# Kernel optimization log

Hardware: AMD Instinct MI355X
Metric: run time of the kernel (lower is better)

Reference implementation:

```python
import jax, jax.numpy as jnp
import numpy as np

B, L, D, H = 64, 2048, 128, 4
A = 128          # atom_dim
M = 16           # num_prototypes
V = 100000       # vocab_size
NNZ = 262144     # total atoms across batch
HD = D // H      # head_dim
GAMMA, BETA, TAU = 0.3, 1.0, 1.0


def setup_inputs() -> dict:
    key = jax.random.key(0)
    ks = jax.random.split(key, 14)
    token_states = jax.random.normal(ks[0], (B, L, D), dtype=jnp.float32)
    query_ids = jax.random.randint(ks[1], (NNZ,), 0, V, dtype=jnp.int64)
    inner = jnp.sort(jax.random.randint(ks[2], (B - 1,), 0, NNZ, dtype=jnp.int64))
    query_offs = jnp.concatenate([jnp.zeros(1, jnp.int64), inner,
                                  jnp.full((1,), NNZ, jnp.int64)])
    atom_emb = jax.random.normal(ks[3], (V, A), dtype=jnp.float32) * 0.02
    phi_logits = jax.random.normal(ks[4], (M, V), dtype=jnp.float32) * 0.02
    W_A = jax.random.normal(ks[5], (A, A), dtype=jnp.float32) * (A ** -0.5)
    W_B = jax.random.normal(ks[6], (A, A), dtype=jnp.float32) * (A ** -0.5)
    W_val = jax.random.normal(ks[7], (HD, A), dtype=jnp.float32) * (A ** -0.5)
    b_val = jax.random.normal(ks[8], (HD,), dtype=jnp.float32) * 0.01
    W_gate = jax.random.normal(ks[9], (H, D), dtype=jnp.float32) * (D ** -0.5)
    b_gate = jax.random.normal(ks[10], (H,), dtype=jnp.float32) * 0.01
    W_out = jax.random.normal(ks[11], (D, D), dtype=jnp.float32) * (D ** -0.5)
    b_out = jax.random.normal(ks[12], (D,), dtype=jnp.float32) * 0.01
    size_w = jax.random.normal(ks[13], (2,), dtype=jnp.float32) * 0.01
    return dict(token_states=token_states, query_ids=query_ids, query_offs=query_offs,
                atom_emb=atom_emb, phi_logits=phi_logits, W_A=W_A, W_B=W_B,
                W_val=W_val, b_val=b_val, W_gate=W_gate, b_gate=b_gate,
                W_out=W_out, b_out=b_out, size_w=size_w)


def reference(token_states, query_ids, query_offs, atom_emb, phi_logits,
              W_A, W_B, W_val, b_val, W_gate, b_gate, W_out, b_out, size_w):
    nB, nL, nD = token_states.shape
    nnz = query_ids.shape[0]
    # segment id for each CSR entry: b s.t. offs[b] <= i < offs[b+1]
    seg = jnp.searchsorted(query_offs[1:], jnp.arange(nnz), side='right')
    # Phi(S) = sum of atom embeddings per set  -> (B, A)
    PhiQ = jax.ops.segment_sum(atom_emb[query_ids], seg, num_segments=nB)
    sizeQ = (query_offs[1:] - query_offs[:-1]).astype(jnp.float32)  # (B,)
    # prototype memberships and features
    p = jax.nn.sigmoid(phi_logits)        # (M, V)
    PhiP = p @ atom_emb                   # (M, A)
    sizeP = p.sum(axis=-1)                # (M,)
    # E[Delta(S,p)] = |S| + |p|_1 - 2 * sum_{u in S} p_u  -> (B, M)
    sum_p_S = jax.ops.segment_sum(p[:, query_ids].T, seg, num_segments=nB)
    delta = sizeQ[:, None] + sizeP[None, :] - 2.0 * sum_p_S
    # attention scores over prototypes
    AQ = PhiQ @ W_A.T                     # (B, A)
    BP = PhiP @ W_B.T                     # (M, A)
    dot = AQ @ BP.T                       # (B, M)
    size_term = size_w[0] * sizeQ[:, None] + size_w[1] * sizeP[None, :]
    scores = -GAMMA * delta + BETA * dot + size_term
    attn = jax.nn.softmax(scores / max(1e-6, TAU), axis=1)   # (B, M)
    Vp = PhiP @ W_val.T + b_val           # (M, HD)
    Z = attn @ Vp                         # (B, HD), shared across heads
    # token->set gates and mixing
    gates = jax.nn.softmax(token_states @ W_gate.T + b_gate, axis=-1)  # (B, L, H)
    mixed = (gates[..., None] * Z[:, None, None, :]).reshape(nB, nL, nD)
    return mixed @ W_out.T + b_out
```

## Files before the change

kernel.cpp:

```cpp
#include <hip/hip_runtime.h>
#include <hip/hip_bf16.h>

constexpr int Bn = 64;
constexpr int Ln = 2048;
constexpr int Dn = 128;
constexpr int Hn = 4;
constexpr int An = 128;
constexpr int Mn = 16;
constexpr int Vn = 100000;
constexpr int HDn = 32;
constexpr float GAMMA = 0.3f;
constexpr float BETA = 1.0f;

constexpr size_t OFF_PHIP  = 0;
constexpr size_t OFF_SIZEP = 2048;
constexpr size_t OFF_PHIQ  = 2064;
constexpr size_t OFF_SUMPS = 10256;
constexpr size_t OFF_C     = 11280;
constexpr size_t OFF_PT    = 44048;
constexpr size_t WS_FLOATS_NEEDED = OFF_PT + (size_t)Vn * 16;

__global__ __launch_bounds__(256) void k_phip(const float* __restrict__ phi,
                                              const float* __restrict__ E,
                                              float* __restrict__ PhiP,
                                              float* __restrict__ sizeP,
                                              float* __restrict__ pT,
                                              int write_pT) {
    __shared__ float pv[64 * 16];
    __shared__ float szl[Mn];
    const int t = threadIdx.x;
    const int a4 = t & 31;
    const int g = t >> 5;
    const int vloc = t >> 2;
    const int mbase = 4 * (t & 3);

    if (t < Mn) szl[t] = 0.f;

    float4 acc0 = make_float4(0.f, 0.f, 0.f, 0.f);
    float4 acc1 = make_float4(0.f, 0.f, 0.f, 0.f);
    float4 szacc = make_float4(0.f, 0.f, 0.f, 0.f);

    for (int v0 = blockIdx.x * 64; v0 < Vn; v0 += gridDim.x * 64) {
        __syncthreads();
        const int v = v0 + vloc;
        float4 pj = make_float4(0.f, 0.f, 0.f, 0.f);
        if (v < Vn) {
            const float x0 = phi[(size_t)(mbase + 0) * Vn + v];
            const float x1 = phi[(size_t)(mbase + 1) * Vn + v];
            const float x2 = phi[(size_t)(mbase + 2) * Vn + v];
            const float x3 = phi[(size_t)(mbase + 3) * Vn + v];
            pj.x = 1.f / (1.f + __expf(-x0));
            pj.y = 1.f / (1.f + __expf(-x1));
            pj.z = 1.f / (1.f + __expf(-x2));
            pj.w = 1.f / (1.f + __expf(-x3));
        }
        *(float4*)&pv[4 * t] = pj;
        szacc.x += pj.x; szacc.y += pj.y; szacc.z += pj.z; szacc.w += pj.w;
        if (write_pT && v < Vn) {
            *(float4*)&pT[(size_t)v * 16 + mbase] = pj;
        }
        __syncthreads();
        const int vmax = min(64, Vn - v0);
#pragma unroll 8
        for (int vv = 0; vv < vmax; ++vv) {
            const float4 e = *(const float4*)&E[(size_t)(v0 + vv) * An + a4 * 4];
            const float2 pm = *(const float2*)&pv[vv * 16 + g * 2];
            acc0.x += pm.x * e.x; acc0.y += pm.x * e.y; acc0.z += pm.x * e.z; acc0.w += pm.x * e.w;
            acc1.x += pm.y * e.x; acc1.y += pm.y * e.y; acc1.z += pm.y * e.z; acc1.w += pm.y * e.w;
        }
    }
    {
        float* d0 = &PhiP[(size_t)(2 * g + 0) * An + a4 * 4];
        float* d1 = &PhiP[(size_t)(2 * g + 1) * An + a4 * 4];
        atomicAdd(d0 + 0, acc0.x); atomicAdd(d0 + 1, acc0.y);
        atomicAdd(d0 + 2, acc0.z); atomicAdd(d0 + 3, acc0.w);
        atomicAdd(d1 + 0, acc1.x); atomicAdd(d1 + 1, acc1.y);
        atomicAdd(d1 + 2, acc1.z); atomicAdd(d1 + 3, acc1.w);
    }
    atomicAdd(&szl[mbase + 0], szacc.x);
    atomicAdd(&szl[mbase + 1], szacc.y);
    atomicAdd(&szl[mbase + 2], szacc.z);
    atomicAdd(&szl[mbase + 3], szacc.w);
    __syncthreads();
    if (t < Mn) atomicAdd(&sizeP[t], szl[t]);
}

__global__ __launch_bounds__(256) void k_phiq(const int* __restrict__ qid,
                                              const int* __restrict__ offs,
                                              const float* __restrict__ E,
                                              const float* __restrict__ phi,
                                              const float* __restrict__ pT,
                                              int usepT,
                                              float* __restrict__ PhiQ,
                                              float* __restrict__ sumpS) {
    const int b = blockIdx.y;
    const int s0 = offs[b], s1 = offs[b + 1];
    const int len = s1 - s0;
    const int nsplit = (int)gridDim.x;
    const int chunk = (len + nsplit - 1) / nsplit;
    const int start = s0 + (int)blockIdx.x * chunk;
    const int end = min(start + chunk, s1);
    const int t = threadIdx.x;

    __shared__ float phl[8 * 128];
    __shared__ float sP[Mn];
    if (t < Mn) sP[t] = 0.f;

    {
        const int a4 = t & 31, sub = t >> 5;
        float4 acc = make_float4(0.f, 0.f, 0.f, 0.f);
        const float4* E4 = (const float4*)E;
        int i = start + sub;
        for (; i + 24 < end; i += 32) {
            const int q0 = qid[i], q1 = qid[i + 8], q2 = qid[i + 16], q3 = qid[i + 24];
            const float4 e0 = E4[(size_t)q0 * 32 + a4];
            const float4 e1 = E4[(size_t)q1 * 32 + a4];
            const float4 e2 = E4[(size_t)q2 * 32 + a4];
            const float4 e3 = E4[(size_t)q3 * 32 + a4];
            acc.x += e0.x + e1.x + e2.x + e3.x;
            acc.y += e0.y + e1.y + e2.y + e3.y;
            acc.z += e0.z + e1.z + e2.z + e3.z;
            acc.w += e0.w + e1.w + e2.w + e3.w;
        }
        for (; i < end; i += 8) {
            const float4 e = E4[(size_t)qid[i] * 32 + a4];
            acc.x += e.x; acc.y += e.y; acc.z += e.z; acc.w += e.w;
        }
        *(float4*)&phl[sub * 128 + a4 * 4] = acc;
    }
    __syncthreads();
    if (t < 128) {
        float s = 0.f;
#pragma unroll
        for (int k = 0; k < 8; ++k) s += phl[k * 128 + t];
        atomicAdd(&PhiQ[(size_t)b * An + t], s);
    }

    float4 acc = make_float4(0.f, 0.f, 0.f, 0.f);
    const int m4 = t & 3, io = t >> 2;
    if (usepT) {
        const float4* pT4 = (const float4*)pT;
        int i = start + io;
        for (; i + 192 < end; i += 256) {
            const int q0 = qid[i], q1 = qid[i + 64], q2 = qid[i + 128], q3 = qid[i + 192];
            const float4 p0 = pT4[(size_t)q0 * 4 + m4];
            const float4 p1 = pT4[(size_t)q1 * 4 + m4];
            const float4 p2 = pT4[(size_t)q2 * 4 + m4];
            const float4 p3 = pT4[(size_t)q3 * 4 + m4];
            acc.x += p0.x + p1.x + p2.x + p3.x;
            acc.y += p0.y + p1.y + p2.y + p3.y;
            acc.z += p0.z + p1.z + p2.z + p3.z;
            acc.w += p0.w + p1.w + p2.w + p3.w;
        }
        for (; i < end; i += 64) {
            const float4 p = pT4[(size_t)qid[i] * 4 + m4];
            acc.x += p.x; acc.y += p.y; acc.z += p.z; acc.w += p.w;
        }
    } else {
        for (int i = start + io; i < end; i += 64) {
            const int q = qid[i];
            acc.x += 1.f / (1.f + __expf(-phi[(size_t)(m4 * 4 + 0) * Vn + q]));
            acc.y += 1.f / (1.f + __expf(-phi[(size_t)(m4 * 4 + 1) * Vn + q]));
            acc.z += 1.f / (1.f + __expf(-phi[(size_t)(m4 * 4 + 2) * Vn + q]));
            acc.w += 1.f / (1.f + __expf(-phi[(size_t)(m4 * 4 + 3) * Vn + q]));
        }
    }
#pragma unroll
    for (int off = 32; off >= 4; off >>= 1) {
        acc.x += __shfl_xor(acc.x, off);
        acc.y += __shfl_xor(acc.y, off);
        acc.z += __shfl_xor(acc.z, off);
        acc.w += __shfl_xor(acc.w, off);
    }
    if ((t & 63) < 4) {
        atomicAdd(&sP[m4 * 4 + 0], acc.x);
        atomicAdd(&sP[m4 * 4 + 1], acc.y);
        atomicAdd(&sP[m4 * 4 + 2], acc.z);
        atomicAdd(&sP[m4 * 4 + 3], acc.w);
    }
    __syncthreads();
    if (t < Mn) atomicAdd(&sumpS[(size_t)b * Mn + t], sP[t]);
}

__global__ __launch_bounds__(128) void k_small(const float* __restrict__ PhiP,
                                               const float* __restrict__ sizeP,
                                               const float* __restrict__ PhiQ,
                                               const float* __restrict__ sumpS,
                                               const int* __restrict__ offs,
                                               const float* __restrict__ W_A,
                                               const float* __restrict__ W_B,
                                               const float* __restrict__ W_val,
                                               const float* __restrict__ b_val,
                                               const float* __restrict__ W_out,
                                               const float* __restrict__ size_w,
                                               float* __restrict__ Cws) {
    const int b = blockIdx.x;
    const int i = threadIdx.x;
    __shared__ float BP[Mn * An];
    __shared__ float Vp[Mn * HDn];
    __shared__ float AQs[An];
    __shared__ float sc[Mn];
    __shared__ float attn[Mn];
    __shared__ float Zs[HDn];

    {
        const float4* wa = (const float4*)(W_A + (size_t)i * An);
        const float4* pq = (const float4*)(PhiQ + (size_t)b * An);
        float aq = 0.f;
        for (int q = 0; q < An / 4; ++q) {
            const float4 w = wa[q], p = pq[q];
            aq += w.x * p.x + w.y * p.y + w.z * p.z + w.w * p.w;
        }
        AQs[i] = aq;
    }
    {
        const float4* wb = (const float4*)(W_B + (size_t)i * An);
        for (int m = 0; m < Mn; ++m) {
            const float4* pp = (const float4*)(PhiP + (size_t)m * An);
            float s = 0.f;
            for (int q = 0; q < An / 4; ++q) {
                const float4 w = wb[q], p = pp[q];
                s += w.x * p.x + w.y * p.y + w.z * p.z + w.w * p.w;
            }
            BP[m * An + i] = s;
        }
    }
    if (i < HDn) {
        const float4* wv = (const float4*)(W_val + (size_t)i * An);
        for (int m = 0; m < Mn; ++m) {
            const float4* pp = (const float4*)(PhiP + (size_t)m * An);
            float s = 0.f;
            for (int q = 0; q < An / 4; ++q) {
                const float4 w = wv[q], p = pp[q];
                s += w.x * p.x + w.y * p.y + w.z * p.z + w.w * p.w;
            }
            Vp[m * HDn + i] = s + b_val[i];
        }
    }
    __syncthreads();

    const float szQ = (float)(offs[b + 1] - offs[b]);
    if (i < Mn) {
        float d = 0.f;
        for (int a = 0; a < An; ++a) d += AQs[a] * BP[i * An + a];
        const float delta = szQ + sizeP[i] - 2.f * sumpS[(size_t)b * Mn + i];
        sc[i] = -GAMMA * delta + BETA * d + size_w[0] * szQ + size_w[1] * sizeP[i];
    }
    __syncthreads();
    if (i < Mn) {
        float mx = sc[0];
        for (int m = 1; m < Mn; ++m) mx = fmaxf(mx, sc[m]);
        float sum = 0.f;
        for (int m = 0; m < Mn; ++m) sum += __expf(sc[m] - mx);
        attn[i] = __expf(sc[i] - mx) / sum;
    }
    __syncthreads();
    if (i < HDn) {
        float z = 0.f;
        for (int m = 0; m < Mn; ++m) z += attn[m] * Vp[m * HDn + i];
        Zs[i] = z;
    }
    __syncthreads();
    {
        const float* wo = W_out + (size_t)i * Dn;
#pragma unroll
        for (int h = 0; h < Hn; ++h) {
            float c = 0.f;
#pragma unroll
            for (int j = 0; j < HDn; ++j) c += Zs[j] * wo[h * HDn + j];
            Cws[((size_t)b * Hn + h) * Dn + i] = c;
        }
    }
}

__global__ __launch_bounds__(256) void k_out(const float* __restrict__ ts,
                                             const float* __restrict__ W_gate,
                                             const float* __restrict__ b_gate,
                                             const float* __restrict__ b_out,
                                             const float* __restrict__ Cws,
                                             float* __restrict__ out) {
    constexpr int CHUNK = 128;
    const int b = blockIdx.y;
    const int t = threadIdx.x;
    __shared__ float4 WgS[Hn * 32];
    __shared__ float4 CS[Hn * 32];
    __shared__ float4 boS[32];
    __shared__ float bgS[Hn];
    if (t < 128) WgS[t] = ((const float4*)W_gate)[t];
    else CS[t - 128] = ((const float4*)(Cws + (size_t)b * Hn * Dn))[t - 128];
    if (t < 32) boS[t] = ((const float4*)b_out)[t];
    if (t >= 64 && t < 64 + Hn) bgS[t - 64] = b_gate[t - 64];
    __syncthreads();

    const int sl = t & 31;
    const int tg = t >> 5;
    const size_t rowbase = (size_t)b * Ln + (size_t)blockIdx.x * CHUNK;
    const float4* x4 = (const float4*)ts + rowbase * 32;
    float4* o4 = (float4*)out + rowbase * 32;

    const float4 w0 = WgS[0 * 32 + sl], w1 = WgS[1 * 32 + sl];
    const float4 w2 = WgS[2 * 32 + sl], w3 = WgS[3 * 32 + sl];
    const float4 c0 = CS[0 * 32 + sl], c1 = CS[1 * 32 + sl];
    const float4 c2 = CS[2 * 32 + sl], c3 = CS[3 * 32 + sl];
    const float4 bo = boS[sl];
    const float bg0 = bgS[0], bg1 = bgS[1], bg2 = bgS[2], bg3 = bgS[3];

    for (int it = 0; it < CHUNK / 8; ++it) {
        const int tok = it * 8 + tg;
        const float4 x = x4[(size_t)tok * 32 + sl];
        float a0 = x.x * w0.x + x.y * w0.y + x.z * w0.z + x.w * w0.w;
        float a1 = x.x * w1.x + x.y * w1.y + x.z * w1.z + x.w * w1.w;
        float a2 = x.x * w2.x + x.y * w2.y + x.z * w2.z + x.w * w2.w;
        float a3 = x.x * w3.x + x.y * w3.y + x.z * w3.z + x.w * w3.w;
#pragma unroll
        for (int off = 16; off > 0; off >>= 1) {
            a0 += __shfl_xor(a0, off);
            a1 += __shfl_xor(a1, off);
            a2 += __shfl_xor(a2, off);
            a3 += __shfl_xor(a3, off);
        }
        a0 += bg0; a1 += bg1; a2 += bg2; a3 += bg3;
        const float mx = fmaxf(fmaxf(a0, a1), fmaxf(a2, a3));
        const float e0 = __expf(a0 - mx), e1 = __expf(a1 - mx);
        const float e2 = __expf(a2 - mx), e3 = __expf(a3 - mx);
        const float inv = 1.f / (e0 + e1 + e2 + e3);
        const float g0 = e0 * inv, g1 = e1 * inv, g2 = e2 * inv, g3 = e3 * inv;
        float4 o = bo;
        o.x += g0 * c0.x + g1 * c1.x + g2 * c2.x + g3 * c3.x;
        o.y += g0 * c0.y + g1 * c1.y + g2 * c2.y + g3 * c3.y;
        o.z += g0 * c0.z + g1 * c1.z + g2 * c2.z + g3 * c3.z;
        o.w += g0 * c0.w + g1 * c1.w + g2 * c2.w + g3 * c3.w;
        o4[(size_t)tok * 32 + sl] = o;
    }
}

extern "C" void kernel_launch(void* const* d_in, const int* in_sizes, int n_in,
                              void* d_out, int out_size, void* d_ws, size_t ws_size,
                              hipStream_t stream) {
    const float* ts     = (const float*)d_in[0];
    const int*   qid    = (const int*)d_in[1];
    const int*   offs   = (const int*)d_in[2];
    const float* E      = (const float*)d_in[3];
    const float* phi    = (const float*)d_in[4];
    const float* W_A    = (const float*)d_in[5];
    const float* W_B    = (const float*)d_in[6];
    const float* W_val  = (const float*)d_in[7];
    const float* b_val  = (const float*)d_in[8];
    const float* W_gate = (const float*)d_in[9];
    const float* b_gate = (const float*)d_in[10];
    const float* W_out  = (const float*)d_in[11];
    const float* b_out  = (const float*)d_in[12];
    const float* size_w = (const float*)d_in[13];
    float* out = (float*)d_out;
    float* ws  = (float*)d_ws;

    float* PhiP  = ws + OFF_PHIP;
    float* sizeP = ws + OFF_SIZEP;
    float* PhiQ  = ws + OFF_PHIQ;
    float* sumpS = ws + OFF_SUMPS;
    float* Cws   = ws + OFF_C;
    float* pT    = ws + OFF_PT;
    const int usepT = (ws_size >= WS_FLOATS_NEEDED * sizeof(float)) ? 1 : 0;

    hipMemsetAsync(ws, 0, OFF_C * sizeof(float), stream);
    k_phip<<<dim3(512), dim3(256), 0, stream>>>(phi, E, PhiP, sizeP, pT, usepT);
    k_phiq<<<dim3(64, Bn), dim3(256), 0, stream>>>(qid, offs, E, phi, pT, usepT, PhiQ, sumpS);
    k_small<<<dim3(Bn), dim3(128), 0, stream>>>(PhiP, sizeP, PhiQ, sumpS, offs,
                                                W_A, W_B, W_val, b_val, W_out, size_w, Cws);
    k_out<<<dim3(Ln / 128, Bn), dim3(256), 0, stream>>>(ts, W_gate, b_gate, b_out, Cws, out);
}
```

Baseline: 322.4 us.

## Restructure PhiP kernel: one 128-vocab tile per block, all prototypes per thread

The prototype-embedding kernel now launches one block per 128-row vocab tile instead of a grid-stride loop over 512 blocks. Each thread accumulates all 16 prototypes against one float4 of the embedding row, so each embedding load is reused 16 times instead of 2. Partial sums are reduced through shuffles and shared memory, then written to global memory with atomics. This cuts redundant embedding reads and per-iteration barriers, but uses 64 accumulator registers per thread and issues far more global atomics from about 782 blocks.

```diff
diff --git a/kernel.cpp b/kernel.cpp
--- a/kernel.cpp
+++ b/kernel.cpp
@@ -20,68 +20,127 @@
 constexpr size_t OFF_PT    = 44048;
 constexpr size_t WS_FLOATS_NEEDED = OFF_PT + (size_t)Vn * 16;
 
+__device__ __forceinline__ float sigm(float x) { return 1.f / (1.f + __expf(-x)); }
+
 __global__ __launch_bounds__(256) void k_phip(const float* __restrict__ phi,
                                               const float* __restrict__ E,
                                               float* __restrict__ PhiP,
                                               float* __restrict__ sizeP,
                                               float* __restrict__ pT,
                                               int write_pT) {
-    __shared__ float pv[64 * 16];
+    __shared__ float pv[128 * 16];
+    __shared__ float4 red[4 * Mn * 32];
     __shared__ float szl[Mn];
     const int t = threadIdx.x;
+    const int v0 = (int)blockIdx.x * 128;
+    const int nvalid = min(128, Vn - v0);
+
+    if (t < Mn) szl[t] = 0.f;
+    __syncthreads();
+
+    {
+        const int vl = t >> 1;
+        const int mb = 8 * (t & 1);
+        float4 p0 = make_float4(0.f, 0.f, 0.f, 0.f);
+        float4 p1 = make_float4(0.f, 0.f, 0.f, 0.f);
+        if (vl < nvalid) {
+            const int v = v0 + vl;
+            p0.x = sigm(phi[(size_t)(mb + 0) * Vn + v]);
+            p0.y = sigm(phi[(size_t)(mb + 1) * Vn + v]);
+            p0.z = sigm(phi[(size_t)(mb + 2) * Vn + v]);
+            p0.w = sigm(phi[(size_t)(mb + 3) * Vn + v]);
+            p1.x = sigm(phi[(size_t)(mb + 4) * Vn + v]);
+            p1.y = sigm(phi[(size_t)(mb + 5) * Vn + v]);
+            p1.z = sigm(phi[(size_t)(mb + 6) * Vn + v]);
+            p1.w = sigm(phi[(size_t)(mb + 7) * Vn + v]);
+            if (write_pT) {
+                *(float4*)&pT[(size_t)v * 16 + mb + 0] = p0;
+                *(float4*)&pT[(size_t)v * 16 + mb + 4] = p1;
+            }
+            atomicAdd(&szl[mb + 0], p0.x); atomicAdd(&szl[mb + 1], p0.y);
+            atomicAdd(&szl[mb + 2], p0.z); atomicAdd(&szl[mb + 3], p0.w);
+            atomicAdd(&szl[mb + 4], p1.x); atomicAdd(&szl[mb + 5], p1.y);
+            atomicAdd(&szl[mb + 6], p1.z); atomicAdd(&szl[mb + 7], p1.w);
+        }
+        *(float4*)&pv[vl * 16 + mb + 0] = p0;
+        *(float4*)&pv[vl * 16 + mb + 4] = p1;
+    }
+    __syncthreads();
+
     const int a4 = t & 31;
-    const int g = t >> 5;
-    const int vloc = t >> 2;
-    const int mbase = 4 * (t & 3);
-
-    if (t < Mn) szl[t] = 0.f;
-
-    float4 acc0 = make_float4(0.f, 0.f, 0.f, 0.f);
-    float4 acc1 = make_float4(0.f, 0.f, 0.f, 0.f);
-    float4 szacc = make_float4(0.f, 0.f, 0.f, 0.f);
-
-    for (int v0 = blockIdx.x * 64; v0 < Vn; v0 += gridDim.x * 64) {
-        __syncthreads();
-        const int v = v0 + vloc;
-        float4 pj = make_float4(0.f, 0.f, 0.f, 0.f);
-        if (v < Vn) {
-            const float x0 = phi[(size_t)(mbase + 0) * Vn + v];
-            const float x1 = phi[(size_t)(mbase + 1) * Vn + v];
-            const float x2 = phi[(size_t)(mbase + 2) * Vn + v];
-            const float x3 = phi[(size_t)(mbase + 3) * Vn + v];
-            pj.x = 1.f / (1.f + __expf(-x0));
-            pj.y = 1.f / (1.f + __expf(-x1));
-            pj.z = 1.f / (1.f + __expf(-x2));
-            pj.w = 1.f / (1.f + __expf(-x3));
-        }
-        *(float4*)&pv[4 * t] = pj;
-        szacc.x += pj.x; szacc.y += pj.y; szacc.z += pj.z; szacc.w += pj.w;
-        if (write_pT && v < Vn) {
-            *(float4*)&pT[(size_t)v * 16 + mbase] = pj;
-        }
-        __syncthreads();
-        const int vmax = min(64, Vn - v0);
-#pragma unroll 8
-        for (int vv = 0; vv < vmax; ++vv) {
-            const float4 e = *(const float4*)&E[(size_t)(v0 + vv) * An + a4 * 4];
-            const float2 pm = *(const float2*)&pv[vv * 16 + g * 2];
-            acc0.x += pm.x * e.x; acc0.y += pm.x * e.y; acc0.z += pm.x * e.z; acc0.w += pm.x * e.w;
-            acc1.x += pm.y * e.x; acc1.y += pm.y * e.y; acc1.z += pm.y * e.z; acc1.w += pm.y * e.w;
-        }
-    }
-    {
-        float* d0 = &PhiP[(size_t)(2 * g + 0) * An + a4 * 4];
-        float* d1 = &PhiP[(size_t)(2 * g + 1) * An + a4 * 4];
-        atomicAdd(d0 + 0, acc0.x); atomicAdd(d0 + 1, acc0.y);
-        atomicAdd(d0 + 2, acc0.z); atomicAdd(d0 + 3, acc0.w);
-        atomicAdd(d1 + 0, acc1.x); atomicAdd(d1 + 1, acc1.y);
-        atomicAdd(d1 + 2, acc1.z); atomicAdd(d1 + 3, acc1.w);
-    }
-    atomicAdd(&szl[mbase + 0], szacc.x);
-    atomicAdd(&szl[mbase + 1], szacc.y);
-    atomicAdd(&szl[mbase + 2], szacc.z);
-    atomicAdd(&szl[mbase + 3], szacc.w);
-    __syncthreads();
+    const int sub = t >> 5;
+    float4 acc[Mn];
+#pragma unroll
+    for (int m = 0; m < Mn; ++m) acc[m] = make_float4(0.f, 0.f, 0.f, 0.f);
+
+    const float4* E4 = (const float4*)E + (size_t)v0 * 32 + a4;
+    if (nvalid == 128) {
+#pragma unroll 4
+        for (int v = sub; v < 128; v += 8) {
+            const float4 e = E4[(size_t)v * 32];
+            const float4 q0 = *(const float4*)&pv[v * 16 + 0];
+            const float4 q1 = *(const float4*)&pv[v * 16 + 4];
+            const float4 q2 = *(const float4*)&pv[v * 16 + 8];
+            const float4 q3 = *(const float4*)&pv[v * 16 + 12];
+            acc[0].x += q0.x * e.x; acc[0].y += q0.x * e.y; acc[0].z += q0.x * e.z; acc[0].w += q0.x * e.w;
+            acc[1].x += q0.y * e.x; acc[1].y += q0.y * e.y; acc[1].z += q0.y * e.z; acc[1].w += q0.y * e.w;
+            acc[2].x += q0.z * e.x; acc[2].y += q0.z * e.y; acc[2].z += q0.z * e.z; acc[2].w += q0.z * e.w;
+            acc[3].x += q0.w * e.x; acc[3].y += q0.w * e.y; acc[3].z += q0.w * e.z; acc[3].w += q0.w * e.w;
+            acc[4].x += q1.x * e.x; acc[4].y += q1.x * e.y; acc[4].z += q1.x * e.z; acc[4].w += q1.x * e.w;
+            acc[5].x += q1.y * e.x; acc[5].y += q1.y * e.y; acc[5].z += q1.y * e.z; acc[5].w += q1.y * e.w;
+            acc[6].x += q1.z * e.x; acc[6].y += q1.z * e.y; acc[6].z += q1.z * e.z; acc[6].w += q1.z * e.w;
+            acc[7].x += q1.w * e.x; acc[7].y += q1.w * e.y; acc[7].z += q1.w * e.z; acc[7].w += q1.w * e.w;
+            acc[8].x += q2.x * e.x; acc[8].y += q2.x * e.y; acc[8].z += q2.x * e.z; acc[8].w += q2.x * e.w;
+            acc[9].x += q2.y * e.x; acc[9].y += q2.y * e.y; acc[9].z += q2.y * e.z; acc[9].w += q2.y * e.w;
+            acc[10].x += q2.z * e.x; acc[10].y += q2.z * e.y; acc[10].z += q2.z * e.z; acc[10].w += q2.z * e.w;
+            acc[11].x += q2.w * e.x; acc[11].y += q2.w * e.y; acc[11].z += q2.w * e.z; acc[11].w += q2.w * e.w;
+            acc[12].x += q3.x * e.x; acc[12].y += q3.x * e.y; acc[12].z += q3.x * e.z; acc[12].w += q3.x * e.w;
+            acc[13].x += q3.y * e.x; acc[13].y += q3.y * e.y; acc[13].z += q3.y * e.z; acc[13].w += q3.y * e.w;
+            acc[14].x += q3.z * e.x; acc[14].y += q3.z * e.y; acc[14].z += q3.z * e.z; acc[14].w += q3.z * e.w;
+            acc[15].x += q3.w * e.x; acc[15].y += q3.w * e.y; acc[15].z += q3.w * e.z; acc[15].w += q3.w * e.w;
+        }
+    } else {
+        for (int v = sub; v < nvalid; v += 8) {
+            const float4 e = E4[(size_t)v * 32];
+#pragma unroll
+            for (int m = 0; m < Mn; ++m) {
+                const float pm = pv[v * 16 + m];
+                acc[m].x += pm * e.x; acc[m].y += pm * e.y;
+                acc[m].z += pm * e.z; acc[m].w += pm * e.w;
+            }
+        }
+    }
+    __syncthreads();
+
+#pragma unroll
+    for (int m = 0; m < Mn; ++m) {
+        acc[m].x += __shfl_xor(acc[m].x, 32);
+        acc[m].y += __shfl_xor(acc[m].y, 32);
+        acc[m].z += __shfl_xor(acc[m].z, 32);
+        acc[m].w += __shfl_xor(acc[m].w, 32);
+    }
+    const int lane = t & 63, wv = t >> 6;
+    if (lane < 32) {
+#pragma unroll
+        for (int m = 0; m < Mn; ++m)
+            red[(wv * Mn + m) * 32 + a4] = acc[m];
+    }
+    __syncthreads();
+
+#pragma unroll
+    for (int r = 0; r < 2; ++r) {
+        const int idx = t + r * 256;
+        const int m = idx >> 5, a = idx & 31;
+        const float4 s0 = red[(0 * Mn + m) * 32 + a];
+        const float4 s1 = red[(1 * Mn + m) * 32 + a];
+        const float4 s2 = red[(2 * Mn + m) * 32 + a];
+        const float4 s3 = red[(3 * Mn + m) * 32 + a];
+        float* dst = &PhiP[(size_t)m * An + a * 4];
+        atomicAdd(dst + 0, s0.x + s1.x + s2.x + s3.x);
+        atomicAdd(dst + 1, s0.y + s1.y + s2.y + s3.y);
+        atomicAdd(dst + 2, s0.z + s1.z + s2.z + s3.z);
+        atomicAdd(dst + 3, s0.w + s1.w + s2.w + s3.w);
+    }
     if (t < Mn) atomicAdd(&sizeP[t], szl[t]);
 }
 
@@ -159,10 +218,10 @@
     } else {
         for (int i = start + io; i < end; i += 64) {
             const int q = qid[i];
-            acc.x += 1.f / (1.f + __expf(-phi[(size_t)(m4 * 4 + 0) * Vn + q]));
-            acc.y += 1.f / (1.f + __expf(-phi[(size_t)(m4 * 4 + 1) * Vn + q]));
-            acc.z += 1.f / (1.f + __expf(-phi[(size_t)(m4 * 4 + 2) * Vn + q]));
-            acc.w += 1.f / (1.f + __expf(-phi[(size_t)(m4 * 4 + 3) * Vn + q]));
+            acc.x += sigm(phi[(size_t)(m4 * 4 + 0) * Vn + q]);
+            acc.y += sigm(phi[(size_t)(m4 * 4 + 1) * Vn + q]);
+            acc.z += sigm(phi[(size_t)(m4 * 4 + 2) * Vn + q]);
+            acc.w += sigm(phi[(size_t)(m4 * 4 + 3) * Vn + q]);
         }
     }
 #pragma unroll
@@ -363,7 +422,7 @@
     const int usepT = (ws_size >= WS_FLOATS_NEEDED * sizeof(float)) ? 1 : 0;
 
     hipMemsetAsync(ws, 0, OFF_C * sizeof(float), stream);
-    k_phip<<<dim3(512), dim3(256), 0, stream>>>(phi, E, PhiP, sizeP, pT, usepT);
+    k_phip<<<dim3((Vn + 127) / 128), dim3(256), 0, stream>>>(phi, E, PhiP, sizeP, pT, usepT);
     k_phiq<<<dim3(64, Bn), dim3(256), 0, stream>>>(qid, offs, E, phi, pT, usepT, PhiQ, sumpS);
     k_small<<<dim3(Bn), dim3(128), 0, stream>>>(PhiP, sizeP, PhiQ, sumpS, offs,
                                                 W_A, W_B, W_val, b_val, W_out, size_w, Cws);
```

Result: slower. 347.3 us (+7.7%).

## Split PhiP into sigmoid-transpose pass and register-tiled GEMV with partial reduction

Applied to the files above, without the earlier changes.

The fused sigmoid+PhiP kernel becomes three kernels. k_pt computes sigmoid and writes the transposed p table plus sizeP. k_phip streams atom_emb once, keeping all 16 prototype accumulators in registers with software prefetch, and writes per-block partials. k_red reduces those partials, replacing the many global atomics of the old kernel. This costs extra launches, heavy register use, and an 8 MB partial buffer write and read; an atomic path is kept if the workspace is too small.

```diff
diff --git a/kernel.cpp b/kernel.cpp
--- a/kernel.cpp
+++ b/kernel.cpp
@@ -12,20 +12,147 @@
 constexpr float GAMMA = 0.3f;
 constexpr float BETA = 1.0f;
 
+constexpr int PHIP_BLOCKS = 1024;
+
 constexpr size_t OFF_PHIP  = 0;
 constexpr size_t OFF_SIZEP = 2048;
 constexpr size_t OFF_PHIQ  = 2064;
 constexpr size_t OFF_SUMPS = 10256;
 constexpr size_t OFF_C     = 11280;
 constexpr size_t OFF_PT    = 44048;
-constexpr size_t WS_FLOATS_NEEDED = OFF_PT + (size_t)Vn * 16;
-
-__global__ __launch_bounds__(256) void k_phip(const float* __restrict__ phi,
-                                              const float* __restrict__ E,
-                                              float* __restrict__ PhiP,
-                                              float* __restrict__ sizeP,
-                                              float* __restrict__ pT,
-                                              int write_pT) {
+constexpr size_t OFF_PART  = OFF_PT + (size_t)Vn * 16;
+constexpr size_t WS_FLOATS_PT   = OFF_PART;
+constexpr size_t WS_FLOATS_PART = OFF_PART + (size_t)PHIP_BLOCKS * Mn * An;
+
+__device__ __forceinline__ float sigm(float x) { return 1.f / (1.f + __expf(-x)); }
+
+__global__ __launch_bounds__(256) void k_pt(const float* __restrict__ phi,
+                                            float* __restrict__ pT,
+                                            float* __restrict__ sizeP) {
+    __shared__ float szl[Mn];
+    const int t = threadIdx.x;
+    if (t < Mn) szl[t] = 0.f;
+    __syncthreads();
+    const int v = (int)blockIdx.x * 256 + t;
+    if (v < Vn) {
+        float p[Mn];
+#pragma unroll
+        for (int m = 0; m < Mn; ++m) p[m] = sigm(phi[(size_t)m * Vn + v]);
+        float4* dst = (float4*)&pT[(size_t)v * 16];
+        dst[0] = make_float4(p[0], p[1], p[2], p[3]);
+        dst[1] = make_float4(p[4], p[5], p[6], p[7]);
+        dst[2] = make_float4(p[8], p[9], p[10], p[11]);
+        dst[3] = make_float4(p[12], p[13], p[14], p[15]);
+#pragma unroll
+        for (int m = 0; m < Mn; ++m) atomicAdd(&szl[m], p[m]);
+    }
+    __syncthreads();
+    if (t < Mn) atomicAdd(&sizeP[t], szl[t]);
+}
+
+__global__ __launch_bounds__(256, 4) void k_phip(const float* __restrict__ E,
+                                                 const float* __restrict__ pT,
+                                                 float* __restrict__ PhiP,
+                                                 float* __restrict__ part,
+                                                 int mode) {
+    const int t = threadIdx.x;
+    const int wv = t >> 6, lane = t & 63;
+    const int c = lane & 31;
+    const int rh = lane >> 5;
+    const int W = (int)gridDim.x * 4;
+    const int w = (int)blockIdx.x * 4 + wv;
+    constexpr int NP = Vn / 2;
+
+    const float4* E4 = (const float4*)E;
+    const float4* P4 = (const float4*)pT;
+
+    float4 acc[Mn];
+#pragma unroll
+    for (int m = 0; m < Mn; ++m) acc[m] = make_float4(0.f, 0.f, 0.f, 0.f);
+
+    int i = w;
+    float4 e_n = make_float4(0.f, 0.f, 0.f, 0.f);
+    float4 pf_n0 = e_n, pf_n1 = e_n, pf_n2 = e_n, pf_n3 = e_n;
+    if (i < NP) {
+        const size_t vr = (size_t)(2 * i + rh);
+        e_n = E4[vr * 32 + c];
+        pf_n0 = P4[vr * 4 + 0]; pf_n1 = P4[vr * 4 + 1];
+        pf_n2 = P4[vr * 4 + 2]; pf_n3 = P4[vr * 4 + 3];
+    }
+    while (i < NP) {
+        const float4 e = e_n;
+        const float4 f0 = pf_n0, f1 = pf_n1, f2 = pf_n2, f3 = pf_n3;
+        const int in = i + W;
+        if (in < NP) {
+            const size_t vr = (size_t)(2 * in + rh);
+            e_n = E4[vr * 32 + c];
+            pf_n0 = P4[vr * 4 + 0]; pf_n1 = P4[vr * 4 + 1];
+            pf_n2 = P4[vr * 4 + 2]; pf_n3 = P4[vr * 4 + 3];
+        }
+        float pm[Mn];
+        pm[0] = f0.x; pm[1] = f0.y; pm[2] = f0.z; pm[3] = f0.w;
+        pm[4] = f1.x; pm[5] = f1.y; pm[6] = f1.z; pm[7] = f1.w;
+        pm[8] = f2.x; pm[9] = f2.y; pm[10] = f2.z; pm[11] = f2.w;
+        pm[12] = f3.x; pm[13] = f3.y; pm[14] = f3.z; pm[15] = f3.w;
+#pragma unroll
+        for (int m = 0; m < Mn; ++m) {
+            acc[m].x += pm[m] * e.x; acc[m].y += pm[m] * e.y;
+            acc[m].z += pm[m] * e.z; acc[m].w += pm[m] * e.w;
+        }
+        i = in;
+    }
+
+#pragma unroll
+    for (int m = 0; m < Mn; ++m) {
+        acc[m].x += __shfl_xor(acc[m].x, 32);
+        acc[m].y += __shfl_xor(acc[m].y, 32);
+        acc[m].z += __shfl_xor(acc[m].z, 32);
+        acc[m].w += __shfl_xor(acc[m].w, 32);
+    }
+    __shared__ float4 red[4 * Mn * 32];
+    if (lane < 32) {
+#pragma unroll
+        for (int m = 0; m < Mn; ++m) red[(wv * Mn + m) * 32 + c] = acc[m];
+    }
+    __syncthreads();
+#pragma unroll
+    for (int r = 0; r < 2; ++r) {
+        const int idx = t + r * 256;
+        const int m = idx >> 5, a = idx & 31;
+        const float4 s0 = red[(0 * Mn + m) * 32 + a];
+        const float4 s1 = red[(1 * Mn + m) * 32 + a];
+        const float4 s2 = red[(2 * Mn + m) * 32 + a];
+        const float4 s3 = red[(3 * Mn + m) * 32 + a];
+        const float4 s = make_float4(s0.x + s1.x + s2.x + s3.x,
+                                     s0.y + s1.y + s2.y + s3.y,
+                                     s0.z + s1.z + s2.z + s3.z,
+                                     s0.w + s1.w + s2.w + s3.w);
+        if (mode == 0) {
+            ((float4*)part)[(size_t)blockIdx.x * 512 + idx] = s;
+        } else {
+            float* dst = &PhiP[(size_t)m * An + a * 4];
+            atomicAdd(dst + 0, s.x); atomicAdd(dst + 1, s.y);
+            atomicAdd(dst + 2, s.z); atomicAdd(dst + 3, s.w);
+        }
+    }
+}
+
+__global__ __launch_bounds__(128) void k_red(const float* __restrict__ part,
+                                             float* __restrict__ PhiP) {
+    const int m = blockIdx.x;
+    const int kc = blockIdx.y;
+    const int a = threadIdx.x;
+    constexpr int KCH = PHIP_BLOCKS / 8;
+    float s = 0.f;
+    const float* src = part + (size_t)kc * KCH * (Mn * An) + (size_t)m * An + a;
+    for (int k = 0; k < KCH; ++k) s += src[(size_t)k * (Mn * An)];
+    atomicAdd(&PhiP[(size_t)m * An + a], s);
+}
+
+__global__ __launch_bounds__(256) void k_phip_fb(const float* __restrict__ phi,
+                                                 const float* __restrict__ E,
+                                                 float* __restrict__ PhiP,
+                                                 float* __restrict__ sizeP) {
     __shared__ float pv[64 * 16];
     __shared__ float szl[Mn];
     const int t = threadIdx.x;
@@ -45,20 +172,13 @@
         const int v = v0 + vloc;
         float4 pj = make_float4(0.f, 0.f, 0.f, 0.f);
         if (v < Vn) {
-            const float x0 = phi[(size_t)(mbase + 0) * Vn + v];
-            const float x1 = phi[(size_t)(mbase + 1) * Vn + v];
-            const float x2 = phi[(size_t)(mbase + 2) * Vn + v];
-            const float x3 = phi[(size_t)(mbase + 3) * Vn + v];
-            pj.x = 1.f / (1.f + __expf(-x0));
-            pj.y = 1.f / (1.f + __expf(-x1));
-            pj.z = 1.f / (1.f + __expf(-x2));
-            pj.w = 1.f / (1.f + __expf(-x3));
+            pj.x = sigm(phi[(size_t)(mbase + 0) * Vn + v]);
+            pj.y = sigm(phi[(size_t)(mbase + 1) * Vn + v]);
+            pj.z = sigm(phi[(size_t)(mbase + 2) * Vn + v]);
+            pj.w = sigm(phi[(size_t)(mbase + 3) * Vn + v]);
         }
         *(float4*)&pv[4 * t] = pj;
         szacc.x += pj.x; szacc.y += pj.y; szacc.z += pj.z; szacc.w += pj.w;
-        if (write_pT && v < Vn) {
-            *(float4*)&pT[(size_t)v * 16 + mbase] = pj;
-        }
         __syncthreads();
         const int vmax = min(64, Vn - v0);
 #pragma unroll 8
@@ -159,10 +279,10 @@
     } else {
         for (int i = start + io; i < end; i += 64) {
             const int q = qid[i];
-            acc.x += 1.f / (1.f + __expf(-phi[(size_t)(m4 * 4 + 0) * Vn + q]));
-            acc.y += 1.f / (1.f + __expf(-phi[(size_t)(m4 * 4 + 1) * Vn + q]));
-            acc.z += 1.f / (1.f + __expf(-phi[(size_t)(m4 * 4 + 2) * Vn + q]));
-            acc.w += 1.f / (1.f + __expf(-phi[(size_t)(m4 * 4 + 3) * Vn + q]));
+            acc.x += sigm(phi[(size_t)(m4 * 4 + 0) * Vn + q]);
+            acc.y += sigm(phi[(size_t)(m4 * 4 + 1) * Vn + q]);
+            acc.z += sigm(phi[(size_t)(m4 * 4 + 2) * Vn + q]);
+            acc.w += sigm(phi[(size_t)(m4 * 4 + 3) * Vn + q]);
         }
     }
 #pragma unroll
@@ -360,10 +480,20 @@
     float* sumpS = ws + OFF_SUMPS;
     float* Cws   = ws + OFF_C;
     float* pT    = ws + OFF_PT;
-    const int usepT = (ws_size >= WS_FLOATS_NEEDED * sizeof(float)) ? 1 : 0;
+    float* part  = ws + OFF_PART;
+    const int usepT   = (ws_size >= WS_FLOATS_PT * sizeof(float)) ? 1 : 0;
+    const int usePart = (ws_size >= WS_FLOATS_PART * sizeof(float)) ? 1 : 0;
 
     hipMemsetAsync(ws, 0, OFF_C * sizeof(float), stream);
-    k_phip<<<dim3(512), dim3(256), 0, stream>>>(phi, E, PhiP, sizeP, pT, usepT);
+    if (usepT) {
+        k_pt<<<dim3((Vn + 255) / 256), dim3(256), 0, stream>>>(phi, pT, sizeP);
+        k_phip<<<dim3(PHIP_BLOCKS), dim3(256), 0, stream>>>(E, pT, PhiP, part,
+                                                            usePart ? 0 : 1);
+        if (usePart)
+            k_red<<<dim3(Mn, 8), dim3(128), 0, stream>>>(part, PhiP);
+    } else {
+        k_phip_fb<<<dim3(512), dim3(256), 0, stream>>>(phi, E, PhiP, sizeP);
+    }
     k_phiq<<<dim3(64, Bn), dim3(256), 0, stream>>>(qid, offs, E, phi, pT, usepT, PhiQ, sumpS);
     k_small<<<dim3(Bn), dim3(128), 0, stream>>>(PhiP, sizeP, PhiQ, sumpS, offs,
                                                 W_A, W_B, W_val, b_val, W_out, size_w, Cws);
```

Measured after the change: 316.5 us. Within noise of the previous version (-1.8%).
